# Optimization experiments

Measured on AMD Instinct MI355X. Metric: run time of the kernel, lower is better.

## Reference

```python
import jax, jax.numpy as jnp
import numpy as np

EPS = 1e-08
SIGMA = 0.1
B = 1.0


def setup_inputs() -> dict:
    key = jax.random.key(0)
    k1, k2 = jax.random.split(key)
    N, C, H, W = 4, 256, 64, 64
    featureT = jax.random.normal(k1, (N, C, H, W), dtype=jnp.float32)
    featureI = jax.random.normal(k2, (N, C, H, W), dtype=jnp.float32)
    return {"featureT": featureT, "featureI": featureI}


def reference(featureT, featureI):
    N, C, H, W = featureT.shape
    # center both by target mean over (batch, spatial)
    meanT = featureT.mean(axis=(0, 2, 3), keepdims=True)
    fI = featureI - meanT
    fT = featureT - meanT
    # channel-wise L2 normalize
    fI = fI / (jnp.linalg.norm(fI, axis=1, keepdims=True) + EPS)
    fT = fT / (jnp.linalg.norm(fT, axis=1, keepdims=True) + EPS)
    # 1x1-patch conv2d == contraction over channels: sim[n, p, h, w]
    # where p indexes the flattened H*W spatial positions of the target.
    fT_flat = fT.reshape(N, C, H * W)  # [N, C, P]
    sim = jnp.einsum('nchw,ncp->nphw', fI, fT_flat)  # [N, P, H, W]
    raw_dist = (1.0 - sim) / 2.0
    # relative distances: divide by min over patch axis
    div = jnp.min(raw_dist, axis=1, keepdims=True)
    relative_dist = raw_dist / (div + EPS)
    # contextual similarity: exp-weight + sum-normalize over patch axis
    Wt = jnp.exp((B - relative_dist) / (SIGMA + EPS))
    W_sum = Wt.sum(axis=1, keepdims=True)
    CX = Wt / (W_sum + EPS)
    # max over spatial dims of featureI, mean over patches, -log, mean over batch
    CX = CX.max(axis=(2, 3))           # [N, P]
    CX = CX.mean(axis=1)               # [N]
    CX_loss = -jnp.log(CX + EPS)
    return jnp.mean(CX_loss)
```

## Files before the change

kernel.cpp:

```cpp
#include <hip/hip_runtime.h>
#include <cmath>


#define NB 4
#define CC 256
#define HW 4096
#define NQ0 8
#define NP1 32

static constexpr float kEPS = 1e-8f;
static constexpr float kSIG = 0.1f + 1e-8f;

typedef __attribute__((ext_vector_type(8)))  short short8;
typedef __attribute__((ext_vector_type(16))) float f32x16;

enum {
  OFF_MEAN = 0,
  OFF_CMAX = 256,
  OFF_WSUM = OFF_CMAX + NQ0*NB*HW,
  OFF_MAXV = OFF_WSUM + NP1*NB*HW,
  OFF_GB   = OFF_MAXV + NB*HW,
  OFF_GT   = OFF_GB + 2*NB*HW,
  OFF_GI   = OFF_GT + NB*HW*CC/2,
  OFF_S    = OFF_GI + NB*HW*CC/2,
  WS_FLOATS_FULL = OFF_S + NB*HW*HW/2
};

__device__ __forceinline__ ushort cvt_bf16(float x) {
  unsigned u = __float_as_uint(x);
  unsigned r = (u + 0x7fffu + ((u >> 16) & 1u)) >> 16;
  return (ushort)r;
}
__device__ __forceinline__ float bf2f(ushort u) {
  return __uint_as_float((unsigned)u << 16);
}

__device__ __forceinline__ float blockSum256(float v) {
  __shared__ float sh[4];
  const int lane = threadIdx.x & 63, wv = threadIdx.x >> 6;
  #pragma unroll
  for (int o = 32; o > 0; o >>= 1) v += __shfl_down(v, o, 64);
  __syncthreads();
  if (lane == 0) sh[wv] = v;
  __syncthreads();
  return sh[0] + sh[1] + sh[2] + sh[3];
}

__global__ __launch_bounds__(256) void k_mean9(const float* __restrict__ fT,
                                               float* __restrict__ ws) {
  const int c = blockIdx.x, t = threadIdx.x;
  float s = 0.f;
  for (int n = 0; n < NB; ++n) {
    const float* p = fT + (size_t)(n*CC + c)*HW;
    #pragma unroll
    for (int k = 0; k < 16; ++k) s += p[k*256 + t];
  }
  const float tot = blockSum256(s);
  if (t == 0) ws[OFF_MEAN + c] = tot * (1.0f/16384.0f);
}

__global__ __launch_bounds__(256) void k_prep9(const float* __restrict__ fT,
                                               const float* __restrict__ fI,
                                               float* __restrict__ ws) {
  __shared__ float stage[32][257];
  __shared__ float prt[8][32];
  __shared__ float sinv[32];
  const int t = threadIdx.x, l = t & 63;
  int bid = blockIdx.x;
  const int tensor = (bid >= 512); bid &= 511;
  const int n   = bid >> 7;
  const int r32 = bid & 127;
  const int p0  = r32 * 32;

  const float* __restrict__ src = tensor ? fI : fT;
  ushort* __restrict__ dst = (ushort*)(ws + (tensor ? OFF_GI : OFF_GT));
  const float* __restrict__ mean = ws + OFF_MEAN;

  const int pl = t & 31, cg = t >> 5;
  float acc = 0.f;
  #pragma unroll
  for (int i = 0; i < 32; ++i) {
    const int c = cg*32 + i;
    const float v = src[((size_t)(n*CC + c))*HW + p0 + pl] - mean[c];
    stage[pl][c] = v;
    acc += v*v;
  }
  prt[cg][pl] = acc;
  __syncthreads();
  if (t < 32) {
    float s = 0.f;
    #pragma unroll
    for (int g = 0; g < 8; ++g) s += prt[g][t];
    sinv[t] = 1.0f/(sqrtf(s) + kEPS);
  }
  __syncthreads();

  const int w = t >> 6, lhi = l >> 5, m = l & 31;
  const float iv = sinv[m];
  #pragma unroll
  for (int i = 0; i < 4; ++i) {
    const int kc = w*4 + i;
    const int cb = kc*16 + lhi*8;
    short8 o;
    #pragma unroll
    for (int j = 0; j < 8; ++j)
      ((ushort*)&o)[j] = cvt_bf16(stage[m][cb + j] * iv);
    *(short8*)(dst + (((size_t)(n*128 + r32)*16 + kc) << 9) + l*8) = o;
  }
}

__global__ __launch_bounds__(256, 4) void k_gemm9(
    const ushort* __restrict__ gA, const ushort* __restrict__ gB,
    float* __restrict__ ws)
{
  __shared__ ushort Ab[8192];
  __shared__ ushort Eb[32*136];
  __shared__ float red2[128];

  const int t = threadIdx.x;
  const int w = t >> 6, l = t & 63;
  const int ln31 = l & 31, lhi = l >> 5;

  const int b = blockIdx.x;
  const int h = b & 7, sid = b >> 3;
  const int n = sid >> 5;
  const int col0 = (sid & 31) * 128;

  const ushort* __restrict__ gAn = gA + (size_t)(n*128 + h*16)*8192;

  short8 pf[4];
  #pragma unroll
  for (int i = 0; i < 4; ++i)
    pf[i] = *(const short8*)(gAn + (size_t)(i*256 + t)*8);

  const int RB = (col0 >> 5) + w;
  short8 breg[16];
  #pragma unroll
  for (int kc = 0; kc < 16; ++kc)
    breg[kc] = *(const short8*)(gB +
        (((size_t)(n*128 + RB)*16 + kc) << 9) + l*8);

  ushort* __restrict__ Sn = (ushort*)(ws + OFF_S) + (size_t)n*HW*HW;

  const int ecol = w*32 + ln31;
  const int rrow = t >> 4;
  const int rq   = (t & 15) * 8;

  float runl = -3.0e38f;

  for (int iter = 0; iter < 16; ++iter) {
    __syncthreads();
    #pragma unroll
    for (int i = 0; i < 4; ++i)
      *(short8*)&Ab[(i*256 + t)*8] = pf[i];
    if (iter + 1 < 16) {
      const ushort* __restrict__ src = gAn + (size_t)(iter + 1)*8192;
      #pragma unroll
      for (int i = 0; i < 4; ++i)
        pf[i] = *(const short8*)(src + (size_t)(i*256 + t)*8);
    }
    __syncthreads();

    f32x16 acc;
    #pragma unroll
    for (int e = 0; e < 16; ++e) acc[e] = 0.f;
    #pragma unroll
    for (int kc = 0; kc < 16; ++kc) {
      const short8 a0 = *(const short8*)&Ab[kc*512 + l*8];
      acc = __builtin_amdgcn_mfma_f32_32x32x16_bf16(a0, breg[kc], acc, 0, 0, 0);
    }

    #pragma unroll
    for (int r = 0; r < 16; ++r) {
      const int lrow = 4*lhi + (r & 3) + 8*(r >> 2);
      const ushort u = cvt_bf16(acc[r]);
      Eb[lrow*136 + ecol] = u;
      runl = fmaxf(runl, bf2f(u));
    }
    __syncthreads();

    const int pb = h*512 + iter*32;
    #pragma unroll
    for (int k = 0; k < 2; ++k) {
      const int lr = rrow + 16*k;
      const short8 v = *(const short8*)&Eb[lr*136 + rq];
      *(short8*)(Sn + (size_t)(pb + lr)*HW + col0 + rq) = v;
    }
  }

  {
    const float o = __shfl_xor(runl, 32, 64);
    runl = fmaxf(runl, o);
  }
  if (l < 32) red2[w*32 + ln31] = runl;
  __syncthreads();
  if (t < 128)
    ws[OFF_CMAX + h*(NB*HW) + n*HW + col0 + t] = red2[t];
}

__global__ __launch_bounds__(256) void k_pass1(float* __restrict__ ws) {
  const int t = threadIdx.x;
  const int b = blockIdx.x;
  const int pc = b & 31, rest = b >> 5;
  const int n = rest >> 3, qblk = rest & 7;
  const int q = qblk*512 + 2*t;

  float a0, b0, a1, b1;
  {
    float cm0 = -3.0e38f, cm1 = -3.0e38f;
    #pragma unroll
    for (int hh = 0; hh < NQ0; ++hh) {
      cm0 = fmaxf(cm0, ws[OFF_CMAX + hh*(NB*HW) + n*HW + q]);
      cm1 = fmaxf(cm1, ws[OFF_CMAX + hh*(NB*HW) + n*HW + q + 1]);
    }
    const float i0 = 1.0f/(2.0f*(0.5f*(1.0f - cm0) + kEPS));
    const float i1 = 1.0f/(2.0f*(0.5f*(1.0f - cm1) + kEPS));
    b0 = i0 / kSIG; a0 = (1.0f - i0) / kSIG;
    b1 = i1 / kSIG; a1 = (1.0f - i1) / kSIG;
  }

  const ushort* __restrict__ S =
      (const ushort*)(ws + OFF_S) + (size_t)n*HW*HW + q;
  float acc0 = 0.f, acc1 = 0.f;
  const int p0 = pc*128;
  #pragma unroll 8
  for (int i = 0; i < 128; ++i) {
    const ushort2 u = *(const ushort2*)(S + (size_t)(p0 + i)*HW);
    acc0 += __expf(fmaf(b0, bf2f(u.x), a0));
    acc1 += __expf(fmaf(b1, bf2f(u.y), a1));
  }
  float2 o; o.x = acc0; o.y = acc1;
  *(float2*)&ws[OFF_WSUM + pc*(NB*HW) + n*HW + q] = o;
}

__global__ __launch_bounds__(256) void k_gb9(float* __restrict__ ws) {
  const int idx = blockIdx.x*256 + threadIdx.x;
  float cm = -3.0e38f;
  #pragma unroll
  for (int hh = 0; hh < NQ0; ++hh)
    cm = fmaxf(cm, ws[OFF_CMAX + hh*(NB*HW) + idx]);
  const float inv2d = 1.0f/(2.0f*(0.5f*(1.0f - cm) + kEPS));
  const float beta  = inv2d / kSIG;
  const float alpha = (1.0f - inv2d) / kSIG;
  float sw = 0.f;
  #pragma unroll
  for (int pc = 0; pc < NP1; ++pc)
    sw += ws[OFF_WSUM + pc*(NB*HW) + idx];
  ws[OFF_GB + idx]         = alpha - logf(sw + kEPS);
  ws[OFF_GB + NB*HW + idx] = beta;
}

__global__ __launch_bounds__(256) void k_pass2(float* __restrict__ ws) {
  __shared__ float gq[4096], bq[4096];
  const int t = threadIdx.x, w = t >> 6, l = t & 63;
  const int b = blockIdx.x;
  const int n = b >> 8, pg = b & 255;

  const float* __restrict__ G  = ws + OFF_GB + n*HW;
  const float* __restrict__ Bq = ws + OFF_GB + NB*HW + n*HW;
  #pragma unroll
  for (int i = 0; i < 4; ++i) {
    *(float4*)&gq[(i*256 + t)*4] = *(const float4*)&G [(i*256 + t)*4];
    *(float4*)&bq[(i*256 + t)*4] = *(const float4*)&Bq[(i*256 + t)*4];
  }
  __syncthreads();

  const ushort* __restrict__ S =
      (const ushort*)(ws + OFF_S) + (size_t)n*HW*HW;
  #pragma unroll
  for (int r = 0; r < 4; ++r) {
    const int p = pg*16 + w*4 + r;
    const ushort* __restrict__ row = S + (size_t)p*HW;
    float m = -3.0e38f;
    #pragma unroll 4
    for (int it = 0; it < 32; ++it) {
      const int q = it*128 + 2*l;
      const ushort2 u = *(const ushort2*)(row + q);
      m = fmaxf(m, fmaf(bq[q],     bf2f(u.x), gq[q]));
      m = fmaxf(m, fmaf(bq[q + 1], bf2f(u.y), gq[q + 1]));
    }
    #pragma unroll
    for (int o = 32; o > 0; o >>= 1) m = fmaxf(m, __shfl_xor(m, o, 64));
    if (l == 0) ws[OFF_MAXV + n*HW + p] = m;
  }
}

__global__ __launch_bounds__(256) void k_final9(const float* __restrict__ ws,
                                                float* __restrict__ out) {
  const int t = threadIdx.x;
  float loss = 0.f;
  for (int n = 0; n < NB; ++n) {
    float s = 0.f;
    for (int k = 0; k < 16; ++k)
      s += __expf(ws[OFF_MAXV + n*HW + k*256 + t]);
    const float tot = blockSum256(s);
    loss += -logf(tot*(1.0f/4096.0f) + kEPS);
  }
  if (t == 0) out[0] = loss*0.25f;
}

extern "C" void kernel_launch(void* const* d_in, const int* in_sizes, int n_in,
                              void* d_out, int out_size, void* d_ws, size_t ws_size,
                              hipStream_t stream) {
  const float* fT = (const float*)d_in[0];
  const float* fI = (const float*)d_in[1];
  float* out = (float*)d_out;
  float* ws  = (float*)d_ws;

  const size_t need_full = (size_t)WS_FLOATS_FULL * sizeof(float);
  if (ws_size < need_full) return;

  const ushort* GT = (const ushort*)(ws + OFF_GT);
  const ushort* GI = (const ushort*)(ws + OFF_GI);
  k_mean9 <<<256,  256, 0, stream>>>(fT, ws);
  k_prep9 <<<1024, 256, 0, stream>>>(fT, fI, ws);
  k_gemm9 <<<1024, 256, 0, stream>>>(GT, GI, ws);
  k_pass1 <<<1024, 256, 0, stream>>>(ws);
  k_gb9   <<<64,   256, 0, stream>>>(ws);
  k_pass2 <<<1024, 256, 0, stream>>>(ws);
  k_final9<<<1,    256, 0, stream>>>(ws, out);
}
```

Before: 176.5 us.

## Double-buffer GEMM epilogue and widen pass1/pass2 loads to 16-byte vectors

```diff
diff --git a/kernel.cpp b/kernel.cpp
--- a/kernel.cpp
+++ b/kernel.cpp
@@ -114,7 +114,7 @@
     float* __restrict__ ws)
 {
   __shared__ ushort Ab[8192];
-  __shared__ ushort Eb[32*136];
+  __shared__ ushort Eb[2][32*136];
   __shared__ float red2[128];
 
   const int t = threadIdx.x;
@@ -153,13 +153,24 @@
     #pragma unroll
     for (int i = 0; i < 4; ++i)
       *(short8*)&Ab[(i*256 + t)*8] = pf[i];
+    __syncthreads();
+
+    if (iter > 0) {
+      const int pb = h*512 + (iter - 1)*32;
+      const ushort* __restrict__ Ep = &Eb[(iter - 1) & 1][0];
+      #pragma unroll
+      for (int k = 0; k < 2; ++k) {
+        const int lr = rrow + 16*k;
+        const short8 v = *(const short8*)&Ep[lr*136 + rq];
+        *(short8*)(Sn + (size_t)(pb + lr)*HW + col0 + rq) = v;
+      }
+    }
     if (iter + 1 < 16) {
       const ushort* __restrict__ src = gAn + (size_t)(iter + 1)*8192;
       #pragma unroll
       for (int i = 0; i < 4; ++i)
         pf[i] = *(const short8*)(src + (size_t)(i*256 + t)*8);
     }
-    __syncthreads();
 
     f32x16 acc;
     #pragma unroll
@@ -170,20 +181,24 @@
       acc = __builtin_amdgcn_mfma_f32_32x32x16_bf16(a0, breg[kc], acc, 0, 0, 0);
     }
 
+    ushort* __restrict__ Ec = &Eb[iter & 1][0];
     #pragma unroll
     for (int r = 0; r < 16; ++r) {
       const int lrow = 4*lhi + (r & 3) + 8*(r >> 2);
       const ushort u = cvt_bf16(acc[r]);
-      Eb[lrow*136 + ecol] = u;
+      Ec[lrow*136 + ecol] = u;
       runl = fmaxf(runl, bf2f(u));
     }
-    __syncthreads();
-
-    const int pb = h*512 + iter*32;
+  }
+
+  __syncthreads();
+  {
+    const int pb = h*512 + 15*32;
+    const ushort* __restrict__ Ep = &Eb[1][0];
     #pragma unroll
     for (int k = 0; k < 2; ++k) {
       const int lr = rrow + 16*k;
-      const short8 v = *(const short8*)&Eb[lr*136 + rq];
+      const short8 v = *(const short8*)&Ep[lr*136 + rq];
       *(short8*)(Sn + (size_t)(pb + lr)*HW + col0 + rq) = v;
     }
   }
@@ -202,35 +217,51 @@
   const int t = threadIdx.x;
   const int b = blockIdx.x;
   const int pc = b & 31, rest = b >> 5;
-  const int n = rest >> 3, qblk = rest & 7;
-  const int q = qblk*512 + 2*t;
-
-  float a0, b0, a1, b1;
+  const int n = rest >> 1, qh = rest & 1;
+  const int q = qh*2048 + t*8;
+
+  float aa[8], bb[8];
   {
-    float cm0 = -3.0e38f, cm1 = -3.0e38f;
-    #pragma unroll
-    for (int hh = 0; hh < NQ0; ++hh) {
-      cm0 = fmaxf(cm0, ws[OFF_CMAX + hh*(NB*HW) + n*HW + q]);
-      cm1 = fmaxf(cm1, ws[OFF_CMAX + hh*(NB*HW) + n*HW + q + 1]);
-    }
-    const float i0 = 1.0f/(2.0f*(0.5f*(1.0f - cm0) + kEPS));
-    const float i1 = 1.0f/(2.0f*(0.5f*(1.0f - cm1) + kEPS));
-    b0 = i0 / kSIG; a0 = (1.0f - i0) / kSIG;
-    b1 = i1 / kSIG; a1 = (1.0f - i1) / kSIG;
+    float cm[8];
+    {
+      float4 x0 = *(const float4*)&ws[OFF_CMAX + n*HW + q];
+      float4 x1 = *(const float4*)&ws[OFF_CMAX + n*HW + q + 4];
+      cm[0]=x0.x; cm[1]=x0.y; cm[2]=x0.z; cm[3]=x0.w;
+      cm[4]=x1.x; cm[5]=x1.y; cm[6]=x1.z; cm[7]=x1.w;
+    }
+    #pragma unroll
+    for (int hh = 1; hh < NQ0; ++hh) {
+      const float4 y0 = *(const float4*)&ws[OFF_CMAX + hh*(NB*HW) + n*HW + q];
+      const float4 y1 = *(const float4*)&ws[OFF_CMAX + hh*(NB*HW) + n*HW + q + 4];
+      cm[0]=fmaxf(cm[0],y0.x); cm[1]=fmaxf(cm[1],y0.y);
+      cm[2]=fmaxf(cm[2],y0.z); cm[3]=fmaxf(cm[3],y0.w);
+      cm[4]=fmaxf(cm[4],y1.x); cm[5]=fmaxf(cm[5],y1.y);
+      cm[6]=fmaxf(cm[6],y1.z); cm[7]=fmaxf(cm[7],y1.w);
+    }
+    #pragma unroll
+    for (int j = 0; j < 8; ++j) {
+      const float iv = 1.0f/(2.0f*(0.5f*(1.0f - cm[j]) + kEPS));
+      bb[j] = iv / kSIG; aa[j] = (1.0f - iv) / kSIG;
+    }
   }
 
   const ushort* __restrict__ S =
       (const ushort*)(ws + OFF_S) + (size_t)n*HW*HW + q;
-  float acc0 = 0.f, acc1 = 0.f;
+  float acc[8];
+  #pragma unroll
+  for (int j = 0; j < 8; ++j) acc[j] = 0.f;
   const int p0 = pc*128;
-  #pragma unroll 8
+  #pragma unroll 4
   for (int i = 0; i < 128; ++i) {
-    const ushort2 u = *(const ushort2*)(S + (size_t)(p0 + i)*HW);
-    acc0 += __expf(fmaf(b0, bf2f(u.x), a0));
-    acc1 += __expf(fmaf(b1, bf2f(u.y), a1));
-  }
-  float2 o; o.x = acc0; o.y = acc1;
-  *(float2*)&ws[OFF_WSUM + pc*(NB*HW) + n*HW + q] = o;
+    const short8 u = *(const short8*)(S + (size_t)(p0 + i)*HW);
+    #pragma unroll
+    for (int j = 0; j < 8; ++j)
+      acc[j] += __expf(fmaf(bb[j], bf2f(((const ushort*)&u)[j]), aa[j]));
+  }
+  float4 o0; o0.x=acc[0]; o0.y=acc[1]; o0.z=acc[2]; o0.w=acc[3];
+  float4 o1; o1.x=acc[4]; o1.y=acc[5]; o1.z=acc[6]; o1.w=acc[7];
+  *(float4*)&ws[OFF_WSUM + pc*(NB*HW) + n*HW + q]     = o0;
+  *(float4*)&ws[OFF_WSUM + pc*(NB*HW) + n*HW + q + 4] = o1;
 }
 
 __global__ __launch_bounds__(256) void k_gb9(float* __restrict__ ws) {
@@ -251,7 +282,8 @@
 }
 
 __global__ __launch_bounds__(256) void k_pass2(float* __restrict__ ws) {
-  __shared__ float gq[4096], bq[4096];
+  __shared__ float gqp[8*640];
+  __shared__ float bqp[8*640];
   const int t = threadIdx.x, w = t >> 6, l = t & 63;
   const int b = blockIdx.x;
   const int n = b >> 8, pg = b & 255;
@@ -259,29 +291,53 @@
   const float* __restrict__ G  = ws + OFF_GB + n*HW;
   const float* __restrict__ Bq = ws + OFF_GB + NB*HW + n*HW;
   #pragma unroll
-  for (int i = 0; i < 4; ++i) {
-    *(float4*)&gq[(i*256 + t)*4] = *(const float4*)&G [(i*256 + t)*4];
-    *(float4*)&bq[(i*256 + t)*4] = *(const float4*)&Bq[(i*256 + t)*4];
+  for (int pass = 0; pass < 4; ++pass) {
+    const int q = pass*1024 + t*4;
+    const int a = (q >> 9)*640 + ((q >> 3) & 63)*10 + (q & 7);
+    const float4 g  = *(const float4*)&G[q];
+    const float4 bv = *(const float4*)&Bq[q];
+    float2 w0; w0.x=g.x;  w0.y=g.y;  *(float2*)&gqp[a]   = w0;
+    float2 w1; w1.x=g.z;  w1.y=g.w;  *(float2*)&gqp[a+2] = w1;
+    float2 w2; w2.x=bv.x; w2.y=bv.y; *(float2*)&bqp[a]   = w2;
+    float2 w3; w3.x=bv.z; w3.y=bv.w; *(float2*)&bqp[a+2] = w3;
   }
   __syncthreads();
 
   const ushort* __restrict__ S =
       (const ushort*)(ws + OFF_S) + (size_t)n*HW*HW;
+  const int p = pg*16 + w*4;
+
+  float m[4];
+  #pragma unroll
+  for (int r = 0; r < 4; ++r) m[r] = -3.0e38f;
+
+  #pragma unroll 2
+  for (int it = 0; it < 8; ++it) {
+    const int abase = it*640 + l*10;
+    float g[8], bb[8];
+    #pragma unroll
+    for (int k = 0; k < 4; ++k) {
+      const float2 gv = *(const float2*)&gqp[abase + 2*k];
+      const float2 bv = *(const float2*)&bqp[abase + 2*k];
+      g[2*k] = gv.x;  g[2*k+1] = gv.y;
+      bb[2*k] = bv.x; bb[2*k+1] = bv.y;
+    }
+    const int qo = it*512 + l*8;
+    #pragma unroll
+    for (int r = 0; r < 4; ++r) {
+      const short8 u = *(const short8*)(S + (size_t)(p + r)*HW + qo);
+      #pragma unroll
+      for (int j = 0; j < 8; ++j)
+        m[r] = fmaxf(m[r], fmaf(bb[j], bf2f(((const ushort*)&u)[j]), g[j]));
+    }
+  }
+
   #pragma unroll
   for (int r = 0; r < 4; ++r) {
-    const int p = pg*16 + w*4 + r;
-    const ushort* __restrict__ row = S + (size_t)p*HW;
-    float m = -3.0e38f;
-    #pragma unroll 4
-    for (int it = 0; it < 32; ++it) {
-      const int q = it*128 + 2*l;
-      const ushort2 u = *(const ushort2*)(row + q);
-      m = fmaxf(m, fmaf(bq[q],     bf2f(u.x), gq[q]));
-      m = fmaxf(m, fmaf(bq[q + 1], bf2f(u.y), gq[q + 1]));
-    }
-    #pragma unroll
-    for (int o = 32; o > 0; o >>= 1) m = fmaxf(m, __shfl_xor(m, o, 64));
-    if (l == 0) ws[OFF_MAXV + n*HW + p] = m;
+    float mv = m[r];
+    #pragma unroll
+    for (int o = 32; o > 0; o >>= 1) mv = fmaxf(mv, __shfl_xor(mv, o, 64));
+    if (l == 0) ws[OFF_MAXV + n*HW + p + r] = mv;
   }
 }
 
@@ -315,7 +371,7 @@
   k_mean9 <<<256,  256, 0, stream>>>(fT, ws);
   k_prep9 <<<1024, 256, 0, stream>>>(fT, fI, ws);
   k_gemm9 <<<1024, 256, 0, stream>>>(GT, GI, ws);
-  k_pass1 <<<1024, 256, 0, stream>>>(ws);
+  k_pass1 <<<256,  256, 0, stream>>>(ws);
   k_gb9   <<<64,   256, 0, stream>>>(ws);
   k_pass2 <<<1024, 256, 0, stream>>>(ws);
   k_final9<<<1,    256, 0, stream>>>(ws, out);
```

Result: slower. 180.7 us (+2.4%).

## Recompute similarity GEMM in each pass instead of materializing bf16 matrix

Applied to the files above, without the earlier changes.

```diff
diff --git a/kernel.cpp b/kernel.cpp
--- a/kernel.cpp
+++ b/kernel.cpp
@@ -6,7 +6,7 @@
 #define CC 256
 #define HW 4096
 #define NQ0 8
-#define NP1 32
+#define NCS 32
 
 static constexpr float kEPS = 1e-8f;
 static constexpr float kSIG = 0.1f + 1e-8f;
@@ -18,12 +18,12 @@
   OFF_MEAN = 0,
   OFF_CMAX = 256,
   OFF_WSUM = OFF_CMAX + NQ0*NB*HW,
-  OFF_MAXV = OFF_WSUM + NP1*NB*HW,
+  OFF_MAXP = OFF_WSUM + NQ0*NB*HW,
+  OFF_MAXV = OFF_MAXP + NCS*NB*HW,
   OFF_GB   = OFF_MAXV + NB*HW,
   OFF_GT   = OFF_GB + 2*NB*HW,
   OFF_GI   = OFF_GT + NB*HW*CC/2,
-  OFF_S    = OFF_GI + NB*HW*CC/2,
-  WS_FLOATS_FULL = OFF_S + NB*HW*HW/2
+  WS_FLOATS_FULL = OFF_GI + NB*HW*CC/2
 };
 
 __device__ __forceinline__ ushort cvt_bf16(float x) {
@@ -109,17 +109,17 @@
   }
 }
 
-__global__ __launch_bounds__(256, 4) void k_gemm9(
+
+__global__ __launch_bounds__(256, 4) void k_gA(
     const ushort* __restrict__ gA, const ushort* __restrict__ gB,
     float* __restrict__ ws)
 {
   __shared__ ushort Ab[8192];
-  __shared__ ushort Eb[32*136];
   __shared__ float red2[128];
 
   const int t = threadIdx.x;
   const int w = t >> 6, l = t & 63;
-  const int ln31 = l & 31, lhi = l >> 5;
+  const int ln31 = l & 31;
 
   const int b = blockIdx.x;
   const int h = b & 7, sid = b >> 3;
@@ -140,12 +140,6 @@
     breg[kc] = *(const short8*)(gB +
         (((size_t)(n*128 + RB)*16 + kc) << 9) + l*8);
 
-  ushort* __restrict__ Sn = (ushort*)(ws + OFF_S) + (size_t)n*HW*HW;
-
-  const int ecol = w*32 + ln31;
-  const int rrow = t >> 4;
-  const int rq   = (t & 15) * 8;
-
   float runl = -3.0e38f;
 
   for (int iter = 0; iter < 16; ++iter) {
@@ -153,13 +147,13 @@
     #pragma unroll
     for (int i = 0; i < 4; ++i)
       *(short8*)&Ab[(i*256 + t)*8] = pf[i];
+    __syncthreads();
     if (iter + 1 < 16) {
       const ushort* __restrict__ src = gAn + (size_t)(iter + 1)*8192;
       #pragma unroll
       for (int i = 0; i < 4; ++i)
         pf[i] = *(const short8*)(src + (size_t)(i*256 + t)*8);
     }
-    __syncthreads();
 
     f32x16 acc;
     #pragma unroll
@@ -169,68 +163,91 @@
       const short8 a0 = *(const short8*)&Ab[kc*512 + l*8];
       acc = __builtin_amdgcn_mfma_f32_32x32x16_bf16(a0, breg[kc], acc, 0, 0, 0);
     }
-
-    #pragma unroll
-    for (int r = 0; r < 16; ++r) {
-      const int lrow = 4*lhi + (r & 3) + 8*(r >> 2);
-      const ushort u = cvt_bf16(acc[r]);
-      Eb[lrow*136 + ecol] = u;
-      runl = fmaxf(runl, bf2f(u));
-    }
-    __syncthreads();
-
-    const int pb = h*512 + iter*32;
-    #pragma unroll
-    for (int k = 0; k < 2; ++k) {
-      const int lr = rrow + 16*k;
-      const short8 v = *(const short8*)&Eb[lr*136 + rq];
-      *(short8*)(Sn + (size_t)(pb + lr)*HW + col0 + rq) = v;
-    }
-  }
-
-  {
-    const float o = __shfl_xor(runl, 32, 64);
-    runl = fmaxf(runl, o);
-  }
+    #pragma unroll
+    for (int r = 0; r < 16; ++r) runl = fmaxf(runl, acc[r]);
+  }
+
+  runl = fmaxf(runl, __shfl_xor(runl, 32, 64));
   if (l < 32) red2[w*32 + ln31] = runl;
   __syncthreads();
   if (t < 128)
     ws[OFF_CMAX + h*(NB*HW) + n*HW + col0 + t] = red2[t];
 }
 
-__global__ __launch_bounds__(256) void k_pass1(float* __restrict__ ws) {
+__global__ __launch_bounds__(256, 4) void k_gB(
+    const ushort* __restrict__ gA, const ushort* __restrict__ gB,
+    float* __restrict__ ws)
+{
+  __shared__ ushort Ab[8192];
+  __shared__ float red2[128];
+
   const int t = threadIdx.x;
+  const int w = t >> 6, l = t & 63;
+  const int ln31 = l & 31;
+
   const int b = blockIdx.x;
-  const int pc = b & 31, rest = b >> 5;
-  const int n = rest >> 3, qblk = rest & 7;
-  const int q = qblk*512 + 2*t;
-
-  float a0, b0, a1, b1;
+  const int h = b & 7, sid = b >> 3;
+  const int n = sid >> 5;
+  const int col0 = (sid & 31) * 128;
+
+  const int q = col0 + w*32 + ln31;
+  float aq, bq;
   {
-    float cm0 = -3.0e38f, cm1 = -3.0e38f;
-    #pragma unroll
-    for (int hh = 0; hh < NQ0; ++hh) {
-      cm0 = fmaxf(cm0, ws[OFF_CMAX + hh*(NB*HW) + n*HW + q]);
-      cm1 = fmaxf(cm1, ws[OFF_CMAX + hh*(NB*HW) + n*HW + q + 1]);
-    }
-    const float i0 = 1.0f/(2.0f*(0.5f*(1.0f - cm0) + kEPS));
-    const float i1 = 1.0f/(2.0f*(0.5f*(1.0f - cm1) + kEPS));
-    b0 = i0 / kSIG; a0 = (1.0f - i0) / kSIG;
-    b1 = i1 / kSIG; a1 = (1.0f - i1) / kSIG;
-  }
-
-  const ushort* __restrict__ S =
-      (const ushort*)(ws + OFF_S) + (size_t)n*HW*HW + q;
-  float acc0 = 0.f, acc1 = 0.f;
-  const int p0 = pc*128;
-  #pragma unroll 8
-  for (int i = 0; i < 128; ++i) {
-    const ushort2 u = *(const ushort2*)(S + (size_t)(p0 + i)*HW);
-    acc0 += __expf(fmaf(b0, bf2f(u.x), a0));
-    acc1 += __expf(fmaf(b1, bf2f(u.y), a1));
-  }
-  float2 o; o.x = acc0; o.y = acc1;
-  *(float2*)&ws[OFF_WSUM + pc*(NB*HW) + n*HW + q] = o;
+    float cm = -3.0e38f;
+    #pragma unroll
+    for (int hh = 0; hh < NQ0; ++hh)
+      cm = fmaxf(cm, ws[OFF_CMAX + hh*(NB*HW) + n*HW + q]);
+    const float i0 = 1.0f/(2.0f*(0.5f*(1.0f - cm) + kEPS));
+    bq = i0 / kSIG; aq = (1.0f - i0) / kSIG;
+  }
+
+  const ushort* __restrict__ gAn = gA + (size_t)(n*128 + h*16)*8192;
+
+  short8 pf[4];
+  #pragma unroll
+  for (int i = 0; i < 4; ++i)
+    pf[i] = *(const short8*)(gAn + (size_t)(i*256 + t)*8);
+
+  const int RB = (col0 >> 5) + w;
+  short8 breg[16];
+  #pragma unroll
+  for (int kc = 0; kc < 16; ++kc)
+    breg[kc] = *(const short8*)(gB +
+        (((size_t)(n*128 + RB)*16 + kc) << 9) + l*8);
+
+  float wsum = 0.f;
+
+  for (int iter = 0; iter < 16; ++iter) {
+    __syncthreads();
+    #pragma unroll
+    for (int i = 0; i < 4; ++i)
+      *(short8*)&Ab[(i*256 + t)*8] = pf[i];
+    __syncthreads();
+    if (iter + 1 < 16) {
+      const ushort* __restrict__ src = gAn + (size_t)(iter + 1)*8192;
+      #pragma unroll
+      for (int i = 0; i < 4; ++i)
+        pf[i] = *(const short8*)(src + (size_t)(i*256 + t)*8);
+    }
+
+    f32x16 acc;
+    #pragma unroll
+    for (int e = 0; e < 16; ++e) acc[e] = 0.f;
+    #pragma unroll
+    for (int kc = 0; kc < 16; ++kc) {
+      const short8 a0 = *(const short8*)&Ab[kc*512 + l*8];
+      acc = __builtin_amdgcn_mfma_f32_32x32x16_bf16(a0, breg[kc], acc, 0, 0, 0);
+    }
+    #pragma unroll
+    for (int r = 0; r < 16; ++r)
+      wsum += __expf(fmaf(bq, acc[r], aq));
+  }
+
+  wsum += __shfl_xor(wsum, 32, 64);
+  if (l < 32) red2[w*32 + ln31] = wsum;
+  __syncthreads();
+  if (t < 128)
+    ws[OFF_WSUM + h*(NB*HW) + n*HW + col0 + t] = red2[t];
 }
 
 __global__ __launch_bounds__(256) void k_gb9(float* __restrict__ ws) {
@@ -244,45 +261,100 @@
   const float alpha = (1.0f - inv2d) / kSIG;
   float sw = 0.f;
   #pragma unroll
-  for (int pc = 0; pc < NP1; ++pc)
-    sw += ws[OFF_WSUM + pc*(NB*HW) + idx];
+  for (int hh = 0; hh < NQ0; ++hh)
+    sw += ws[OFF_WSUM + hh*(NB*HW) + idx];
   ws[OFF_GB + idx]         = alpha - logf(sw + kEPS);
   ws[OFF_GB + NB*HW + idx] = beta;
 }
 
-__global__ __launch_bounds__(256) void k_pass2(float* __restrict__ ws) {
-  __shared__ float gq[4096], bq[4096];
-  const int t = threadIdx.x, w = t >> 6, l = t & 63;
+__global__ __launch_bounds__(256, 4) void k_gC(
+    const ushort* __restrict__ gA, const ushort* __restrict__ gB,
+    float* __restrict__ ws)
+{
+  __shared__ ushort Ab[8192];
+  __shared__ float Ef[32*132];
+
+  const int t = threadIdx.x;
+  const int w = t >> 6, l = t & 63;
+  const int ln31 = l & 31, lhi = l >> 5;
+
   const int b = blockIdx.x;
-  const int n = b >> 8, pg = b & 255;
-
-  const float* __restrict__ G  = ws + OFF_GB + n*HW;
-  const float* __restrict__ Bq = ws + OFF_GB + NB*HW + n*HW;
-  #pragma unroll
-  for (int i = 0; i < 4; ++i) {
-    *(float4*)&gq[(i*256 + t)*4] = *(const float4*)&G [(i*256 + t)*4];
-    *(float4*)&bq[(i*256 + t)*4] = *(const float4*)&Bq[(i*256 + t)*4];
-  }
-  __syncthreads();
-
-  const ushort* __restrict__ S =
-      (const ushort*)(ws + OFF_S) + (size_t)n*HW*HW;
-  #pragma unroll
-  for (int r = 0; r < 4; ++r) {
-    const int p = pg*16 + w*4 + r;
-    const ushort* __restrict__ row = S + (size_t)p*HW;
+  const int h = b & 7, sid = b >> 3;
+  const int n = sid >> 5;
+  const int cs = sid & 31;
+  const int col0 = cs * 128;
+
+  const int q = col0 + w*32 + ln31;
+  const float gq = ws[OFF_GB + n*HW + q];
+  const float bq = ws[OFF_GB + NB*HW + n*HW + q];
+
+  const ushort* __restrict__ gAn = gA + (size_t)(n*128 + h*16)*8192;
+
+  short8 pf[4];
+  #pragma unroll
+  for (int i = 0; i < 4; ++i)
+    pf[i] = *(const short8*)(gAn + (size_t)(i*256 + t)*8);
+
+  const int RB = (col0 >> 5) + w;
+  short8 breg[16];
+  #pragma unroll
+  for (int kc = 0; kc < 16; ++kc)
+    breg[kc] = *(const short8*)(gB +
+        (((size_t)(n*128 + RB)*16 + kc) << 9) + l*8);
+
+  const int ecol = w*32 + ln31;
+  const int lr = t >> 3, qc = (t & 7) * 16;
+  float* __restrict__ MAXP = ws + OFF_MAXP + (size_t)cs*(NB*HW) + n*HW;
+
+  for (int iter = 0; iter < 16; ++iter) {
+    __syncthreads();
+    #pragma unroll
+    for (int i = 0; i < 4; ++i)
+      *(short8*)&Ab[(i*256 + t)*8] = pf[i];
+    __syncthreads();
+    if (iter + 1 < 16) {
+      const ushort* __restrict__ src = gAn + (size_t)(iter + 1)*8192;
+      #pragma unroll
+      for (int i = 0; i < 4; ++i)
+        pf[i] = *(const short8*)(src + (size_t)(i*256 + t)*8);
+    }
+
+    f32x16 acc;
+    #pragma unroll
+    for (int e = 0; e < 16; ++e) acc[e] = 0.f;
+    #pragma unroll
+    for (int kc = 0; kc < 16; ++kc) {
+      const short8 a0 = *(const short8*)&Ab[kc*512 + l*8];
+      acc = __builtin_amdgcn_mfma_f32_32x32x16_bf16(a0, breg[kc], acc, 0, 0, 0);
+    }
+
+    #pragma unroll
+    for (int r = 0; r < 16; ++r) {
+      const int lrow = 4*lhi + (r & 3) + 8*(r >> 2);
+      Ef[lrow*132 + ecol] = fmaf(bq, acc[r], gq);
+    }
+    __syncthreads();
+
     float m = -3.0e38f;
-    #pragma unroll 4
-    for (int it = 0; it < 32; ++it) {
-      const int q = it*128 + 2*l;
-      const ushort2 u = *(const ushort2*)(row + q);
-      m = fmaxf(m, fmaf(bq[q],     bf2f(u.x), gq[q]));
-      m = fmaxf(m, fmaf(bq[q + 1], bf2f(u.y), gq[q + 1]));
-    }
-    #pragma unroll
-    for (int o = 32; o > 0; o >>= 1) m = fmaxf(m, __shfl_xor(m, o, 64));
-    if (l == 0) ws[OFF_MAXV + n*HW + p] = m;
-  }
+    #pragma unroll
+    for (int k4 = 0; k4 < 4; ++k4) {
+      const float4 v = *(const float4*)&Ef[lr*132 + qc + 4*k4];
+      m = fmaxf(m, fmaxf(fmaxf(v.x, v.y), fmaxf(v.z, v.w)));
+    }
+    m = fmaxf(m, __shfl_xor(m, 1, 64));
+    m = fmaxf(m, __shfl_xor(m, 2, 64));
+    m = fmaxf(m, __shfl_xor(m, 4, 64));
+    if ((t & 7) == 0) MAXP[h*512 + iter*32 + lr] = m;
+  }
+}
+
+__global__ __launch_bounds__(256) void k_red(float* __restrict__ ws) {
+  const int idx = blockIdx.x*256 + threadIdx.x;
+  float m = ws[OFF_MAXP + idx];
+  #pragma unroll
+  for (int cs = 1; cs < NCS; ++cs)
+    m = fmaxf(m, ws[OFF_MAXP + cs*(NB*HW) + idx]);
+  ws[OFF_MAXV + idx] = m;
 }
 
 __global__ __launch_bounds__(256) void k_final9(const float* __restrict__ ws,
@@ -314,9 +386,10 @@
   const ushort* GI = (const ushort*)(ws + OFF_GI);
   k_mean9 <<<256,  256, 0, stream>>>(fT, ws);
   k_prep9 <<<1024, 256, 0, stream>>>(fT, fI, ws);
-  k_gemm9 <<<1024, 256, 0, stream>>>(GT, GI, ws);
-  k_pass1 <<<1024, 256, 0, stream>>>(ws);
+  k_gA    <<<1024, 256, 0, stream>>>(GT, GI, ws);
+  k_gB    <<<1024, 256, 0, stream>>>(GT, GI, ws);
   k_gb9   <<<64,   256, 0, stream>>>(ws);
-  k_pass2 <<<1024, 256, 0, stream>>>(ws);
+  k_gC    <<<1024, 256, 0, stream>>>(GT, GI, ws);
+  k_red   <<<64,   256, 0, stream>>>(ws);
   k_final9<<<1,    256, 0, stream>>>(ws, out);
 }
```

Result: slower. 204.6 us (+15.9%).
